# Optimization experiments

Measured on AMD Instinct MI355X. Metric: run time of the kernel, lower is better.

## Reference

```python
import jax, jax.numpy as jnp
import numpy as np

B, S, E = 4, 4096, 128  # batch, seq_len, embedding_dim (quaternion groups)
D = 4 * E               # flattened feature dim fed to the Linear layers


def setup_inputs() -> dict:
    key = jax.random.key(0)
    ks = jax.random.split(key, 9)
    scale_w = 1.0 / np.sqrt(D).astype(np.float32)
    return {
        "query": jax.random.normal(ks[0], (B, S, E, 4), dtype=jnp.float32),
        "key": jax.random.normal(ks[1], (B, S, E, 4), dtype=jnp.float32),
        "value": jax.random.normal(ks[2], (B, S, E, 4), dtype=jnp.float32),
        "Wq": jax.random.normal(ks[3], (D, D), dtype=jnp.float32) * scale_w,
        "bq": jax.random.normal(ks[4], (D,), dtype=jnp.float32) * 0.01,
        "Wk": jax.random.normal(ks[5], (D, D), dtype=jnp.float32) * scale_w,
        "bk": jax.random.normal(ks[6], (D,), dtype=jnp.float32) * 0.01,
        "Wv": jax.random.normal(ks[7], (D, D), dtype=jnp.float32) * scale_w,
        "bv": jax.random.normal(ks[8], (D,), dtype=jnp.float32) * 0.01,
    }


def reference(query, key, value, Wq, bq, Wk, bk, Wv, bv):
    b, s = query.shape[0], query.shape[1]
    e = query.shape[2]  # embedding_dim
    # flatten quaternion dim: [B,S,E,4] -> [B,S,4E]
    q = query.reshape(b, s, -1)
    k = key.reshape(b, key.shape[1], -1)
    v = value.reshape(b, value.shape[1], -1)
    # torch nn.Linear: x @ W^T + bias
    Q = (q @ Wq.T + bq).reshape(b, s, -1, 4)
    K = (k @ Wk.T + bk).reshape(b, key.shape[1], -1, 4)
    V = (v @ Wv.T + bv).reshape(b, value.shape[1], -1, 4)
    # full QK^T over quaternion-grouped dims: [B,S,S]
    scores = jnp.einsum('bseq,bkeq->bsk', Q, K) / jnp.sqrt(jnp.float32(e))
    weights = jax.nn.softmax(scores, axis=-1)
    # faithful to the source: weights are summed over k and scale V at position s
    output = jnp.einsum('bsk,bseq->bseq', weights, V)
    return output, weights
```

## Files before the change

### kernel.cpp

```cpp
#include <hip/hip_runtime.h>
#include <cstdint>

typedef _Float16 h1;
typedef _Float16 h4 __attribute__((ext_vector_type(4)));
typedef _Float16 h8 __attribute__((ext_vector_type(8)));
typedef float    f4 __attribute__((ext_vector_type(4)));
typedef float    f32x4 __attribute__((ext_vector_type(4)));

#define NB 4
#define SL 4096
#define DD 512
#define MM (NB*SL)
#define SHIFT 12.0f

__global__ __launch_bounds__(256) void convert_all(
    const float* __restrict__ Xq, const float* __restrict__ Xk, const float* __restrict__ Xv,
    const float* __restrict__ Wq, const float* __restrict__ Wk, const float* __restrict__ Wv,
    h1* __restrict__ Xh, h1* __restrict__ Wh)
{
    const int xper = MM*DD/4;
    const int wper = DD*DD/4;
    const int xtot = 3*xper;
    int i = blockIdx.x * 256 + threadIdx.x;
    const float* src;
    h1* dst;
    int j;
    if (i < xtot) {
        int mat = i / xper; j = i - mat*xper;
        src = (mat==0) ? Xq : (mat==1 ? Xk : Xv);
        dst = Xh + (size_t)mat*MM*DD;
    } else {
        int t = i - xtot;
        if (t >= 3*wper) return;
        int mat = t / wper; j = t - mat*wper;
        src = (mat==0) ? Wq : (mat==1 ? Wk : Wv);
        dst = Wh + (size_t)mat*DD*DD;
    }
    f4 v = ((const f4*)src)[j];
    h4 hv;
    hv[0]=(h1)v[0]; hv[1]=(h1)v[1]; hv[2]=(h1)v[2]; hv[3]=(h1)v[3];
    ((h4*)dst)[j] = hv;
}

__device__ __forceinline__ void stage_tile(const h1* __restrict__ gbase,
                                           h1* lds, int w, int l)
{
    #pragma unroll
    for (int j = 0; j < 4; j++) {
        const int cc  = w*4 + j;
        const int row = cc*8 + (l >> 3);
        const int sc  = (l & 7) ^ (l >> 3);
        const h1* src = gbase + (size_t)row * DD + sc*8;
        void* dst = (char*)lds + cc*1024;
        __builtin_amdgcn_global_load_lds(
            (const __attribute__((address_space(1))) uint32_t*)src,
            (__attribute__((address_space(3))) uint32_t*)dst, 16, 0, 0);
    }
}

__device__ __forceinline__ h8 lds_frag(const h1* lds, int row, int lc)
{
    const int chunk = lc ^ (row & 7);
    return *(const h8*)(lds + row*64 + chunk*8);
}

__device__ __forceinline__ void stage_slot32(const h1* __restrict__ gbase,
                                             char* ldsbase, int w, int l)
{
    #pragma unroll
    for (int j = 0; j < 2; j++) {
        const int lc  = j*512 + w*64 + l;
        const int row = lc >> 2;
        const int ch  = lc & 3;
        const int sc  = ch ^ ((row >> 1) & 3);
        const h1* src = gbase + (size_t)row * DD + sc*8;
        __builtin_amdgcn_global_load_lds(
            (const __attribute__((address_space(1))) uint32_t*)src,
            (__attribute__((address_space(3))) uint32_t*)(ldsbase + (size_t)(j*512 + w*64)*16),
            16, 0, 0);
    }
}

__device__ __forceinline__ h8 frag32(const h1* lds, int row, int g)
{
    const int ch = g ^ ((row >> 1) & 3);
    return *(const h8*)(lds + row*32 + ch*8);
}

__device__ __forceinline__ void slab_write16(h1* slab, const float (&vals)[4][4], int g, int c)
{
    #pragma unroll
    for (int i = 0; i < 4; i++)
        #pragma unroll
        for (int nf = 0; nf < 4; nf++)
            slab[(g*4+i)*72 + nf*16 + c] = (h1)vals[i][nf];
}

__device__ __forceinline__ void slab_flush(const h1* slab, int lane, h1* gdst0, int grow)
{
    __builtin_amdgcn_wave_barrier();
    asm volatile("s_waitcnt lgkmcnt(0)" ::: "memory");
    const int rl = lane >> 3, ch = lane & 7;
    h8 v0 = *(const h8*)(slab + rl*72 + ch*8);
    h8 v1 = *(const h8*)(slab + (8+rl)*72 + ch*8);
    *(h8*)(gdst0 + (size_t)rl*grow + ch*8)     = v0;
    *(h8*)(gdst0 + (size_t)(8+rl)*grow + ch*8) = v1;
    __builtin_amdgcn_wave_barrier();
}

__global__ __launch_bounds__(256) void proj_gemm(
    const h1* __restrict__ Xh, const h1* __restrict__ Wh,
    const float* __restrict__ bq, const float* __restrict__ bk, const float* __restrict__ bv,
    h1* __restrict__ Qh, h1* __restrict__ Kh, float* __restrict__ Vout)
{
    const int prj = blockIdx.z;
    const h1* __restrict__ X    = Xh + (size_t)prj * MM * DD;
    const h1* __restrict__ W    = Wh + (size_t)prj * DD * DD;
    const float* __restrict__ bias = (prj==0) ? bq : (prj==1 ? bk : bv);

    const int m0 = blockIdx.y * 128;
    const int n0 = blockIdx.x * 128;

    __shared__ h1 As[128*64];
    __shared__ h1 Bs[128*64];

    const int tid  = threadIdx.x;
    const int lane = tid & 63;
    const int wid  = tid >> 6;
    const int wm = wid >> 1, wn = wid & 1;
    const int g  = lane >> 4, c = lane & 15;

    f32x4 acc[4][4];
    #pragma unroll
    for (int i = 0; i < 4; i++)
        #pragma unroll
        for (int j = 0; j < 4; j++) acc[i][j] = (f32x4){0.f, 0.f, 0.f, 0.f};

    for (int k0 = 0; k0 < DD; k0 += 64) {
        __syncthreads();
        stage_tile(X + (size_t)m0 * DD + k0, As, wid, lane);
        stage_tile(W + (size_t)n0 * DD + k0, Bs, wid, lane);
        __syncthreads();
        #pragma unroll
        for (int kk = 0; kk < 2; kk++) {
            h8 af[4], bf[4];
            #pragma unroll
            for (int mf = 0; mf < 4; mf++) af[mf] = lds_frag(As, wm*64 + mf*16 + c, kk*4 + g);
            #pragma unroll
            for (int nf = 0; nf < 4; nf++) bf[nf] = lds_frag(Bs, wn*64 + nf*16 + c, kk*4 + g);
            #pragma unroll
            for (int mf = 0; mf < 4; mf++)
                #pragma unroll
                for (int nf = 0; nf < 4; nf++)
                    acc[mf][nf] = __builtin_amdgcn_mfma_f32_16x16x32_f16(af[mf], bf[nf], acc[mf][nf], 0, 0, 0);
        }
    }

    float bv4[4];
    #pragma unroll
    for (int nf = 0; nf < 4; nf++) bv4[nf] = bias[n0 + wn*64 + nf*16 + c];

    __syncthreads();

    if (prj < 2) {
        h1* dstbase = (prj == 0) ? Qh : Kh;
        h1* slab = As + wid*1152;
        #pragma unroll
        for (int mf = 0; mf < 4; mf++) {
            float vals[4][4];
            #pragma unroll
            for (int i = 0; i < 4; i++)
                #pragma unroll
                for (int nf = 0; nf < 4; nf++)
                    vals[i][nf] = acc[mf][nf][i] + bv4[nf];
            slab_write16(slab, vals, g, c);
            slab_flush(slab, lane,
                       dstbase + (size_t)(m0 + wm*64 + mf*16)*DD + n0 + wn*64, DD);
        }
    } else {
        #pragma unroll
        for (int mf = 0; mf < 4; mf++) {
            #pragma unroll
            for (int i = 0; i < 4; i++) {
                const int row = m0 + wm*64 + mf*16 + g*4 + i;
                #pragma unroll
                for (int nf = 0; nf < 4; nf++) {
                    const int col = n0 + wn*64 + nf*16 + c;
                    Vout[(size_t)row*DD + col] = acc[mf][nf][i] + bv4[nf];
                }
            }
        }
    }
}

__global__ __launch_bounds__(512) void scores_gemm_8ph(
    const h1* __restrict__ Qh, const h1* __restrict__ Kh,
    h1* __restrict__ Eh,
    float* __restrict__ partial)
{
    const int orig = blockIdx.x;
    const int swz  = (orig & 7) * 128 + (orig >> 3);
    const int b  = swz >> 8;
    const int t_ = swz & 255;
    const int ty = t_ >> 4;
    const int tx = t_ & 15;
    const int m0 = ty * 256;
    const int n0 = tx * 256;
    const h1* __restrict__ Qb = Qh + (size_t)b * SL * DD;
    const h1* __restrict__ Kb = Kh + (size_t)b * SL * DD;

    __shared__ h1 Albuf[4*256*32];
    __shared__ h1 Blbuf[4*256*32];
    const int SLOT_H = 256*32;
    const int SLOT_B = SLOT_H*2;

    const int tid  = threadIdx.x;
    const int lane = tid & 63;
    const int wid  = tid >> 6;
    const int wm = wid >> 2;
    const int wn = wid & 3;
    const int g  = lane >> 4, c = lane & 15;

    f32x4 acc[8][4];
    #pragma unroll
    for (int i = 0; i < 8; i++)
        #pragma unroll
        for (int j = 0; j < 4; j++) acc[i][j] = (f32x4){0.f, 0.f, 0.f, 0.f};

    #pragma unroll
    for (int kt = 0; kt < 3; ++kt) {
        stage_slot32(Qb + (size_t)m0*DD + kt*32, (char*)Albuf + kt*SLOT_B, wid, lane);
        stage_slot32(Kb + (size_t)n0*DD + kt*32, (char*)Blbuf + kt*SLOT_B, wid, lane);
    }
    asm volatile("s_waitcnt vmcnt(8)" ::: "memory");
    __builtin_amdgcn_s_barrier();

    for (int kt = 0; kt < 16; ++kt) {
        const int cur = kt & 3;
        const h1* Abase = Albuf + cur*SLOT_H;
        const h1* Bbase = Blbuf + cur*SLOT_H;

        h8 af[4], bf[4];
        #pragma unroll
        for (int fm = 0; fm < 4; fm++) af[fm] = frag32(Abase, wm*128 + fm*16 + c, g);
        #pragma unroll
        for (int fn = 0; fn < 4; fn++) bf[fn] = frag32(Bbase, wn*64 + fn*16 + c, g);

        if (kt <= 12) {
            const int nk = kt + 3, ns = nk & 3;
            stage_slot32(Qb + (size_t)m0*DD + nk*32, (char*)Albuf + ns*SLOT_B, wid, lane);
            stage_slot32(Kb + (size_t)n0*DD + nk*32, (char*)Blbuf + ns*SLOT_B, wid, lane);
        }

        __builtin_amdgcn_s_barrier();
        asm volatile("s_waitcnt lgkmcnt(0)" ::: "memory");
        __builtin_amdgcn_sched_barrier(0);
        __builtin_amdgcn_s_setprio(1);
        #pragma unroll
        for (int fm = 0; fm < 4; fm++)
            #pragma unroll
            for (int fn = 0; fn < 4; fn++)
                acc[fm][fn] = __builtin_amdgcn_mfma_f32_16x16x32_f16(af[fm], bf[fn], acc[fm][fn], 0, 0, 0);
        __builtin_amdgcn_s_setprio(0);
        __builtin_amdgcn_s_barrier();

        #pragma unroll
        for (int fm = 0; fm < 4; fm++) af[fm] = frag32(Abase, wm*128 + 64 + fm*16 + c, g);

        __builtin_amdgcn_s_barrier();
        asm volatile("s_waitcnt lgkmcnt(0)" ::: "memory");
        __builtin_amdgcn_sched_barrier(0);
        __builtin_amdgcn_s_setprio(1);
        #pragma unroll
        for (int fm = 0; fm < 4; fm++)
            #pragma unroll
            for (int fn = 0; fn < 4; fn++)
                acc[4+fm][fn] = __builtin_amdgcn_mfma_f32_16x16x32_f16(af[fm], bf[fn], acc[4+fm][fn], 0, 0, 0);
        __builtin_amdgcn_s_setprio(0);

        if (kt <= 12)      { asm volatile("s_waitcnt vmcnt(8)" ::: "memory"); }
        else if (kt == 13) { asm volatile("s_waitcnt vmcnt(4)" ::: "memory"); }
        else if (kt == 14) { asm volatile("s_waitcnt vmcnt(0)" ::: "memory"); }
        __builtin_amdgcn_s_barrier();
    }

    const float inv_scale = 0.08838834764831845f;
    h1* slab = Albuf + wid*1152;
    #pragma unroll
    for (int mf = 0; mf < 8; mf++) {
        float vals[4][4];
        #pragma unroll
        for (int i = 0; i < 4; i++) {
            const int row = m0 + wm*128 + mf*16 + g*4 + i;
            float rsum = 0.f;
            #pragma unroll
            for (int nf = 0; nf < 4; nf++) {
                float e = __expf(fmaf(acc[mf][nf][i], inv_scale, -SHIFT));
                vals[i][nf] = e;
                rsum += e;
            }
            #pragma unroll
            for (int off = 1; off < 16; off <<= 1) rsum += __shfl_xor(rsum, off);
            if (c == 0)
                partial[((size_t)b * SL + row) * 64 + tx * 4 + wn] = rsum;
        }
        slab_write16(slab, vals, g, c);
        slab_flush(slab, lane,
                   Eh + ((size_t)b * SL + m0 + wm*128 + mf*16) * SL + n0 + wn*64, SL);
    }
}

__global__ __launch_bounds__(256) void rownorm(
    const float* __restrict__ partial, const h1* __restrict__ Eh,
    float* __restrict__ Wout)
{
    const int row = blockIdx.x;
    const int tid = threadIdx.x;
    __shared__ float sinv;
    if (tid < 64) {
        float s = partial[(size_t)row * 64 + tid];
        #pragma unroll
        for (int off = 32; off > 0; off >>= 1) s += __shfl_xor(s, off);
        if (tid == 0) sinv = 1.0f / s;
    }
    __syncthreads();
    const float s = sinv;
    const h8* er = (const h8*)(Eh + (size_t)row * SL);
    f4* wr = (f4*)(Wout + (size_t)row * SL);
    #pragma unroll
    for (int jj = 0; jj < 2; jj++) {
        const int j = tid + jj*256;
        h8 v = er[j];
        f4 o0, o1;
        #pragma unroll
        for (int x = 0; x < 4; x++) { o0[x] = (float)v[x] * s; o1[x] = (float)v[4+x] * s; }
        wr[2*j]   = o0;
        wr[2*j+1] = o1;
    }
}

extern "C" void kernel_launch(void* const* d_in, const int* in_sizes, int n_in,
                              void* d_out, int out_size, void* d_ws, size_t ws_size,
                              hipStream_t stream)
{
    const float* q  = (const float*)d_in[0];
    const float* k  = (const float*)d_in[1];
    const float* v  = (const float*)d_in[2];
    const float* Wq = (const float*)d_in[3];
    const float* bq = (const float*)d_in[4];
    const float* Wk = (const float*)d_in[5];
    const float* bk = (const float*)d_in[6];
    const float* Wv = (const float*)d_in[7];
    const float* bv = (const float*)d_in[8];

    float* out  = (float*)d_out;
    float* Vout = out;
    float* Wout = out + (size_t)MM * DD;

    char* ws = (char*)d_ws;
    h1* Xh = (h1*)ws;
    h1* Wh = (h1*)(ws + (size_t)3*MM*DD*2);
    h1* Qh = (h1*)((char*)Wh + (size_t)3*DD*DD*2);
    h1* Kh = (h1*)((char*)Qh + (size_t)MM*DD*2);
    float* partial = (float*)((char*)Kh + (size_t)MM*DD*2);
    float* invrow  = (float*)((char*)partial + (size_t)MM*64*4);
    h1* Eh = (h1*)((char*)invrow + (size_t)MM*4);

    const int conv_chunks = (3*MM*DD + 3*DD*DD) / 4;
    convert_all<<<(conv_chunks + 255)/256, 256, 0, stream>>>(q, k, v, Wq, Wk, Wv, Xh, Wh);
    proj_gemm<<<dim3(4, 128, 3), 256, 0, stream>>>(Xh, Wh, bq, bk, bv, Qh, Kh, Vout);
    scores_gemm_8ph<<<1024, 512, 0, stream>>>(Qh, Kh, Eh, partial);
    rownorm<<<MM, 256, 0, stream>>>(partial, Eh, Wout);
}
```

Before: 264.9 us.

## Fuse fp32-to-fp16 activation conversion into projection GEMM and merge scores MFMA phases

Drops the separate conversion pass over the three activation tensors. The projection GEMM now loads fp32 inputs directly, converts them in registers and writes them to a padded LDS tile, which avoids writing and re-reading an fp16 copy. Only the weights are still pre-converted. The scores GEMM also loads all eight A fragments at once and runs a single MFMA phase with fewer barriers, at the cost of higher register pressure. The activation loads now go through registers instead of asynchronous global-to-LDS copies, so each projection block re-reads fp32 X four times across the N tiles.

```diff
diff --git a/kernel.cpp b/kernel.cpp
--- a/kernel.cpp
+++ b/kernel.cpp
@@ -13,33 +13,20 @@
 #define MM (NB*SL)
 #define SHIFT 12.0f
 
-__global__ __launch_bounds__(256) void convert_all(
-    const float* __restrict__ Xq, const float* __restrict__ Xk, const float* __restrict__ Xv,
+__global__ __launch_bounds__(256) void convert_w_kernel(
     const float* __restrict__ Wq, const float* __restrict__ Wk, const float* __restrict__ Wv,
-    h1* __restrict__ Xh, h1* __restrict__ Wh)
-{
-    const int xper = MM*DD/4;
-    const int wper = DD*DD/4;
-    const int xtot = 3*xper;
+    h1* __restrict__ Wh)
+{
+    const int per = DD*DD/4;
     int i = blockIdx.x * 256 + threadIdx.x;
-    const float* src;
-    h1* dst;
-    int j;
-    if (i < xtot) {
-        int mat = i / xper; j = i - mat*xper;
-        src = (mat==0) ? Xq : (mat==1 ? Xk : Xv);
-        dst = Xh + (size_t)mat*MM*DD;
-    } else {
-        int t = i - xtot;
-        if (t >= 3*wper) return;
-        int mat = t / wper; j = t - mat*wper;
-        src = (mat==0) ? Wq : (mat==1 ? Wk : Wv);
-        dst = Wh + (size_t)mat*DD*DD;
-    }
+    if (i >= 3*per) return;
+    int mat = i / per;
+    int j = i - mat*per;
+    const float* src = (mat==0) ? Wq : (mat==1 ? Wk : Wv);
     f4 v = ((const f4*)src)[j];
     h4 hv;
     hv[0]=(h1)v[0]; hv[1]=(h1)v[1]; hv[2]=(h1)v[2]; hv[3]=(h1)v[3];
-    ((h4*)dst)[j] = hv;
+    ((h4*)(Wh + (size_t)mat*DD*DD))[j] = hv;
 }
 
 __device__ __forceinline__ void stage_tile(const h1* __restrict__ gbase,
@@ -109,19 +96,20 @@
 }
 
 __global__ __launch_bounds__(256) void proj_gemm(
-    const h1* __restrict__ Xh, const h1* __restrict__ Wh,
+    const float* __restrict__ Xq, const float* __restrict__ Xk, const float* __restrict__ Xv,
+    const h1* __restrict__ Wh,
     const float* __restrict__ bq, const float* __restrict__ bk, const float* __restrict__ bv,
     h1* __restrict__ Qh, h1* __restrict__ Kh, float* __restrict__ Vout)
 {
     const int prj = blockIdx.z;
-    const h1* __restrict__ X    = Xh + (size_t)prj * MM * DD;
-    const h1* __restrict__ W    = Wh + (size_t)prj * DD * DD;
+    const float* __restrict__ X    = (prj==0) ? Xq : (prj==1 ? Xk : Xv);
+    const h1*    __restrict__ W    = Wh + (size_t)prj * DD * DD;
     const float* __restrict__ bias = (prj==0) ? bq : (prj==1 ? bk : bv);
 
     const int m0 = blockIdx.y * 128;
     const int n0 = blockIdx.x * 128;
 
-    __shared__ h1 As[128*64];
+    __shared__ h1 As[128][72];
     __shared__ h1 Bs[128*64];
 
     const int tid  = threadIdx.x;
@@ -129,6 +117,7 @@
     const int wid  = tid >> 6;
     const int wm = wid >> 1, wn = wid & 1;
     const int g  = lane >> 4, c = lane & 15;
+    const int r  = tid >> 1,  h = tid & 1;
 
     f32x4 acc[4][4];
     #pragma unroll
@@ -138,14 +127,31 @@
 
     for (int k0 = 0; k0 < DD; k0 += 64) {
         __syncthreads();
-        stage_tile(X + (size_t)m0 * DD + k0, As, wid, lane);
         stage_tile(W + (size_t)n0 * DD + k0, Bs, wid, lane);
+        {
+            const f4* src = (const f4*)(X + (size_t)(m0 + r) * DD + k0 + h*32);
+            f4 a0=src[0], a1=src[1], a2=src[2], a3=src[3],
+               a4=src[4], a5=src[5], a6=src[6], a7=src[7];
+            h8 p0, p1, p2, p3;
+            #pragma unroll
+            for (int j = 0; j < 4; j++) {
+                p0[j]=(h1)a0[j]; p0[4+j]=(h1)a1[j];
+                p1[j]=(h1)a2[j]; p1[4+j]=(h1)a3[j];
+                p2[j]=(h1)a4[j]; p2[4+j]=(h1)a5[j];
+                p3[j]=(h1)a6[j]; p3[4+j]=(h1)a7[j];
+            }
+            *(h8*)&As[r][h*32]      = p0;
+            *(h8*)&As[r][h*32 + 8]  = p1;
+            *(h8*)&As[r][h*32 + 16] = p2;
+            *(h8*)&As[r][h*32 + 24] = p3;
+        }
         __syncthreads();
+
         #pragma unroll
         for (int kk = 0; kk < 2; kk++) {
             h8 af[4], bf[4];
             #pragma unroll
-            for (int mf = 0; mf < 4; mf++) af[mf] = lds_frag(As, wm*64 + mf*16 + c, kk*4 + g);
+            for (int mf = 0; mf < 4; mf++) af[mf] = *(const h8*)&As[wm*64 + mf*16 + c][kk*32 + g*8];
             #pragma unroll
             for (int nf = 0; nf < 4; nf++) bf[nf] = lds_frag(Bs, wn*64 + nf*16 + c, kk*4 + g);
             #pragma unroll
@@ -164,7 +170,7 @@
 
     if (prj < 2) {
         h1* dstbase = (prj == 0) ? Qh : Kh;
-        h1* slab = As + wid*1152;
+        h1* slab = &As[0][0] + wid*1152;
         #pragma unroll
         for (int mf = 0; mf < 4; mf++) {
             float vals[4][4];
@@ -193,7 +199,7 @@
     }
 }
 
-__global__ __launch_bounds__(512) void scores_gemm_8ph(
+__global__ __launch_bounds__(512) void scores_gemm(
     const h1* __restrict__ Qh, const h1* __restrict__ Kh,
     h1* __restrict__ Eh,
     float* __restrict__ partial)
@@ -240,9 +246,9 @@
         const h1* Abase = Albuf + cur*SLOT_H;
         const h1* Bbase = Blbuf + cur*SLOT_H;
 
-        h8 af[4], bf[4];
-        #pragma unroll
-        for (int fm = 0; fm < 4; fm++) af[fm] = frag32(Abase, wm*128 + fm*16 + c, g);
+        h8 af[8], bf[4];
+        #pragma unroll
+        for (int fm = 0; fm < 8; fm++) af[fm] = frag32(Abase, wm*128 + fm*16 + c, g);
         #pragma unroll
         for (int fn = 0; fn < 4; fn++) bf[fn] = frag32(Bbase, wn*64 + fn*16 + c, g);
 
@@ -252,30 +258,14 @@
             stage_slot32(Kb + (size_t)n0*DD + nk*32, (char*)Blbuf + ns*SLOT_B, wid, lane);
         }
 
-        __builtin_amdgcn_s_barrier();
         asm volatile("s_waitcnt lgkmcnt(0)" ::: "memory");
         __builtin_amdgcn_sched_barrier(0);
         __builtin_amdgcn_s_setprio(1);
         #pragma unroll
-        for (int fm = 0; fm < 4; fm++)
+        for (int fm = 0; fm < 8; fm++)
             #pragma unroll
             for (int fn = 0; fn < 4; fn++)
                 acc[fm][fn] = __builtin_amdgcn_mfma_f32_16x16x32_f16(af[fm], bf[fn], acc[fm][fn], 0, 0, 0);
-        __builtin_amdgcn_s_setprio(0);
-        __builtin_amdgcn_s_barrier();
-
-        #pragma unroll
-        for (int fm = 0; fm < 4; fm++) af[fm] = frag32(Abase, wm*128 + 64 + fm*16 + c, g);
-
-        __builtin_amdgcn_s_barrier();
-        asm volatile("s_waitcnt lgkmcnt(0)" ::: "memory");
-        __builtin_amdgcn_sched_barrier(0);
-        __builtin_amdgcn_s_setprio(1);
-        #pragma unroll
-        for (int fm = 0; fm < 4; fm++)
-            #pragma unroll
-            for (int fn = 0; fn < 4; fn++)
-                acc[4+fm][fn] = __builtin_amdgcn_mfma_f32_16x16x32_f16(af[fm], bf[fn], acc[4+fm][fn], 0, 0, 0);
         __builtin_amdgcn_s_setprio(0);
 
         if (kt <= 12)      { asm volatile("s_waitcnt vmcnt(8)" ::: "memory"); }
@@ -358,17 +348,15 @@
     float* Wout = out + (size_t)MM * DD;
 
     char* ws = (char*)d_ws;
-    h1* Xh = (h1*)ws;
-    h1* Wh = (h1*)(ws + (size_t)3*MM*DD*2);
-    h1* Qh = (h1*)((char*)Wh + (size_t)3*DD*DD*2);
+    h1* Wh = (h1*)ws;
+    h1* Qh = (h1*)(ws + (size_t)3*DD*DD*2);
     h1* Kh = (h1*)((char*)Qh + (size_t)MM*DD*2);
     float* partial = (float*)((char*)Kh + (size_t)MM*DD*2);
     float* invrow  = (float*)((char*)partial + (size_t)MM*64*4);
     h1* Eh = (h1*)((char*)invrow + (size_t)MM*4);
 
-    const int conv_chunks = (3*MM*DD + 3*DD*DD) / 4;
-    convert_all<<<(conv_chunks + 255)/256, 256, 0, stream>>>(q, k, v, Wq, Wk, Wv, Xh, Wh);
-    proj_gemm<<<dim3(4, 128, 3), 256, 0, stream>>>(Xh, Wh, bq, bk, bv, Qh, Kh, Vout);
-    scores_gemm_8ph<<<1024, 512, 0, stream>>>(Qh, Kh, Eh, partial);
+    convert_w_kernel<<<768, 256, 0, stream>>>(Wq, Wk, Wv, Wh);
+    proj_gemm<<<dim3(4, 128, 3), 256, 0, stream>>>(q, k, v, Wh, bq, bk, bv, Qh, Kh, Vout);
+    scores_gemm<<<1024, 512, 0, stream>>>(Qh, Kh, Eh, partial);
     rownorm<<<MM, 256, 0, stream>>>(partial, Eh, Wout);
 }
```

Measured after the change: 276.7 us. 1.04x slower.

## Make scores GEMM persistent over four tiles and stage V output via LDS

Applied to the files above, without the earlier changes.

The scores GEMM now launches 256 blocks, each looping over four consecutive 256x256 tiles, instead of 1024 blocks. The XCD-aware block swizzle is dropped. Separately, the fp32 V projection epilogue is staged through shared memory, so each row is written with coalesced 16-byte stores instead of scattered scalar ones. The persistent loop is meant to cut launch and tail overhead, but it serializes the prologue and epilogue of each tile, and losing the swizzle may reduce L2 reuse.

```diff
diff --git a/kernel.cpp b/kernel.cpp
--- a/kernel.cpp
+++ b/kernel.cpp
@@ -108,6 +108,30 @@
     __builtin_amdgcn_wave_barrier();
 }
 
+__device__ __forceinline__ void slab_write32(float* slab, const float (&vals)[4][4], int g, int c)
+{
+    #pragma unroll
+    for (int i = 0; i < 4; i++)
+        #pragma unroll
+        for (int nf = 0; nf < 4; nf++)
+            slab[(g*4+i)*68 + nf*16 + c] = vals[i][nf];
+}
+
+__device__ __forceinline__ void slab_flush32(const float* slab, int lane, float* gdst0, int grow)
+{
+    __builtin_amdgcn_wave_barrier();
+    asm volatile("s_waitcnt lgkmcnt(0)" ::: "memory");
+    const int rl = lane >> 3, ch = lane & 7;
+    #pragma unroll
+    for (int half = 0; half < 2; half++) {
+        f4 v0 = *(const f4*)(slab + rl*68     + half*32 + ch*4);
+        f4 v1 = *(const f4*)(slab + (8+rl)*68 + half*32 + ch*4);
+        *(f4*)(gdst0 + (size_t)rl*grow     + half*32 + ch*4) = v0;
+        *(f4*)(gdst0 + (size_t)(8+rl)*grow + half*32 + ch*4) = v1;
+    }
+    __builtin_amdgcn_wave_barrier();
+}
+
 __global__ __launch_bounds__(256) void proj_gemm(
     const h1* __restrict__ Xh, const h1* __restrict__ Wh,
     const float* __restrict__ bq, const float* __restrict__ bk, const float* __restrict__ bv,
@@ -178,36 +202,28 @@
                        dstbase + (size_t)(m0 + wm*64 + mf*16)*DD + n0 + wn*64, DD);
         }
     } else {
+        float* slab32 = (float*)((char*)(wid < 2 ? As : Bs) + (wid & 1)*4352);
         #pragma unroll
         for (int mf = 0; mf < 4; mf++) {
-            #pragma unroll
-            for (int i = 0; i < 4; i++) {
-                const int row = m0 + wm*64 + mf*16 + g*4 + i;
-                #pragma unroll
-                for (int nf = 0; nf < 4; nf++) {
-                    const int col = n0 + wn*64 + nf*16 + c;
-                    Vout[(size_t)row*DD + col] = acc[mf][nf][i] + bv4[nf];
-                }
-            }
-        }
-    }
-}
-
-__global__ __launch_bounds__(512) void scores_gemm_8ph(
+            float vals[4][4];
+            #pragma unroll
+            for (int i = 0; i < 4; i++)
+                #pragma unroll
+                for (int nf = 0; nf < 4; nf++)
+                    vals[i][nf] = acc[mf][nf][i] + bv4[nf];
+            slab_write32(slab32, vals, g, c);
+            slab_flush32(slab32, lane,
+                         Vout + (size_t)(m0 + wm*64 + mf*16)*DD + n0 + wn*64, DD);
+        }
+    }
+}
+
+__global__ __launch_bounds__(512) void scores_gemm(
     const h1* __restrict__ Qh, const h1* __restrict__ Kh,
     h1* __restrict__ Eh,
     float* __restrict__ partial)
 {
-    const int orig = blockIdx.x;
-    const int swz  = (orig & 7) * 128 + (orig >> 3);
-    const int b  = swz >> 8;
-    const int t_ = swz & 255;
-    const int ty = t_ >> 4;
-    const int tx = t_ & 15;
-    const int m0 = ty * 256;
-    const int n0 = tx * 256;
-    const h1* __restrict__ Qb = Qh + (size_t)b * SL * DD;
-    const h1* __restrict__ Kb = Kh + (size_t)b * SL * DD;
+    const int bid = blockIdx.x;
 
     __shared__ h1 Albuf[4*256*32];
     __shared__ h1 Blbuf[4*256*32];
@@ -221,92 +237,106 @@
     const int wn = wid & 3;
     const int g  = lane >> 4, c = lane & 15;
 
-    f32x4 acc[8][4];
-    #pragma unroll
-    for (int i = 0; i < 8; i++)
-        #pragma unroll
-        for (int j = 0; j < 4; j++) acc[i][j] = (f32x4){0.f, 0.f, 0.f, 0.f};
-
-    #pragma unroll
-    for (int kt = 0; kt < 3; ++kt) {
-        stage_slot32(Qb + (size_t)m0*DD + kt*32, (char*)Albuf + kt*SLOT_B, wid, lane);
-        stage_slot32(Kb + (size_t)n0*DD + kt*32, (char*)Blbuf + kt*SLOT_B, wid, lane);
-    }
-    asm volatile("s_waitcnt vmcnt(8)" ::: "memory");
-    __builtin_amdgcn_s_barrier();
-
-    for (int kt = 0; kt < 16; ++kt) {
-        const int cur = kt & 3;
-        const h1* Abase = Albuf + cur*SLOT_H;
-        const h1* Bbase = Blbuf + cur*SLOT_H;
-
-        h8 af[4], bf[4];
-        #pragma unroll
-        for (int fm = 0; fm < 4; fm++) af[fm] = frag32(Abase, wm*128 + fm*16 + c, g);
-        #pragma unroll
-        for (int fn = 0; fn < 4; fn++) bf[fn] = frag32(Bbase, wn*64 + fn*16 + c, g);
-
-        if (kt <= 12) {
-            const int nk = kt + 3, ns = nk & 3;
-            stage_slot32(Qb + (size_t)m0*DD + nk*32, (char*)Albuf + ns*SLOT_B, wid, lane);
-            stage_slot32(Kb + (size_t)n0*DD + nk*32, (char*)Blbuf + ns*SLOT_B, wid, lane);
-        }
-
+    #pragma unroll 1
+    for (int tt = 0; tt < 4; tt++) {
+        const int t_ = bid*4 + tt;
+        const int b  = t_ >> 8;
+        const int ty = (t_ >> 4) & 15;
+        const int tx = t_ & 15;
+        const int m0 = ty * 256;
+        const int n0 = tx * 256;
+        const h1* __restrict__ Qb = Qh + (size_t)b * SL * DD;
+        const h1* __restrict__ Kb = Kh + (size_t)b * SL * DD;
+
+        f32x4 acc[8][4];
+        #pragma unroll
+        for (int i = 0; i < 8; i++)
+            #pragma unroll
+            for (int j = 0; j < 4; j++) acc[i][j] = (f32x4){0.f, 0.f, 0.f, 0.f};
+
+        __syncthreads();
+
+        #pragma unroll
+        for (int kt = 0; kt < 3; ++kt) {
+            stage_slot32(Qb + (size_t)m0*DD + kt*32, (char*)Albuf + kt*SLOT_B, wid, lane);
+            stage_slot32(Kb + (size_t)n0*DD + kt*32, (char*)Blbuf + kt*SLOT_B, wid, lane);
+        }
+        asm volatile("s_waitcnt vmcnt(8)" ::: "memory");
         __builtin_amdgcn_s_barrier();
-        asm volatile("s_waitcnt lgkmcnt(0)" ::: "memory");
-        __builtin_amdgcn_sched_barrier(0);
-        __builtin_amdgcn_s_setprio(1);
-        #pragma unroll
-        for (int fm = 0; fm < 4; fm++)
-            #pragma unroll
-            for (int fn = 0; fn < 4; fn++)
-                acc[fm][fn] = __builtin_amdgcn_mfma_f32_16x16x32_f16(af[fm], bf[fn], acc[fm][fn], 0, 0, 0);
-        __builtin_amdgcn_s_setprio(0);
-        __builtin_amdgcn_s_barrier();
-
-        #pragma unroll
-        for (int fm = 0; fm < 4; fm++) af[fm] = frag32(Abase, wm*128 + 64 + fm*16 + c, g);
-
-        __builtin_amdgcn_s_barrier();
-        asm volatile("s_waitcnt lgkmcnt(0)" ::: "memory");
-        __builtin_amdgcn_sched_barrier(0);
-        __builtin_amdgcn_s_setprio(1);
-        #pragma unroll
-        for (int fm = 0; fm < 4; fm++)
-            #pragma unroll
-            for (int fn = 0; fn < 4; fn++)
-                acc[4+fm][fn] = __builtin_amdgcn_mfma_f32_16x16x32_f16(af[fm], bf[fn], acc[4+fm][fn], 0, 0, 0);
-        __builtin_amdgcn_s_setprio(0);
-
-        if (kt <= 12)      { asm volatile("s_waitcnt vmcnt(8)" ::: "memory"); }
-        else if (kt == 13) { asm volatile("s_waitcnt vmcnt(4)" ::: "memory"); }
-        else if (kt == 14) { asm volatile("s_waitcnt vmcnt(0)" ::: "memory"); }
-        __builtin_amdgcn_s_barrier();
-    }
-
-    const float inv_scale = 0.08838834764831845f;
-    h1* slab = Albuf + wid*1152;
-    #pragma unroll
-    for (int mf = 0; mf < 8; mf++) {
-        float vals[4][4];
-        #pragma unroll
-        for (int i = 0; i < 4; i++) {
-            const int row = m0 + wm*128 + mf*16 + g*4 + i;
-            float rsum = 0.f;
-            #pragma unroll
-            for (int nf = 0; nf < 4; nf++) {
-                float e = __expf(fmaf(acc[mf][nf][i], inv_scale, -SHIFT));
-                vals[i][nf] = e;
-                rsum += e;
+
+        for (int kt = 0; kt < 16; ++kt) {
+            const int cur = kt & 3;
+            const h1* Abase = Albuf + cur*SLOT_H;
+            const h1* Bbase = Blbuf + cur*SLOT_H;
+
+            h8 af[4], bf[4];
+            #pragma unroll
+            for (int fm = 0; fm < 4; fm++) af[fm] = frag32(Abase, wm*128 + fm*16 + c, g);
+            #pragma unroll
+            for (int fn = 0; fn < 4; fn++) bf[fn] = frag32(Bbase, wn*64 + fn*16 + c, g);
+
+            if (kt <= 12) {
+                const int nk = kt + 3, ns = nk & 3;
+                stage_slot32(Qb + (size_t)m0*DD + nk*32, (char*)Albuf + ns*SLOT_B, wid, lane);
+                stage_slot32(Kb + (size_t)n0*DD + nk*32, (char*)Blbuf + ns*SLOT_B, wid, lane);
             }
-            #pragma unroll
-            for (int off = 1; off < 16; off <<= 1) rsum += __shfl_xor(rsum, off);
-            if (c == 0)
-                partial[((size_t)b * SL + row) * 64 + tx * 4 + wn] = rsum;
-        }
-        slab_write16(slab, vals, g, c);
-        slab_flush(slab, lane,
-                   Eh + ((size_t)b * SL + m0 + wm*128 + mf*16) * SL + n0 + wn*64, SL);
+
+            __builtin_amdgcn_s_barrier();
+            asm volatile("s_waitcnt lgkmcnt(0)" ::: "memory");
+            __builtin_amdgcn_sched_barrier(0);
+            __builtin_amdgcn_s_setprio(1);
+            #pragma unroll
+            for (int fm = 0; fm < 4; fm++)
+                #pragma unroll
+                for (int fn = 0; fn < 4; fn++)
+                    acc[fm][fn] = __builtin_amdgcn_mfma_f32_16x16x32_f16(af[fm], bf[fn], acc[fm][fn], 0, 0, 0);
+            __builtin_amdgcn_s_setprio(0);
+            __builtin_amdgcn_s_barrier();
+
+            #pragma unroll
+            for (int fm = 0; fm < 4; fm++) af[fm] = frag32(Abase, wm*128 + 64 + fm*16 + c, g);
+
+            __builtin_amdgcn_s_barrier();
+            asm volatile("s_waitcnt lgkmcnt(0)" ::: "memory");
+            __builtin_amdgcn_sched_barrier(0);
+            __builtin_amdgcn_s_setprio(1);
+            #pragma unroll
+            for (int fm = 0; fm < 4; fm++)
+                #pragma unroll
+                for (int fn = 0; fn < 4; fn++)
+                    acc[4+fm][fn] = __builtin_amdgcn_mfma_f32_16x16x32_f16(af[fm], bf[fn], acc[4+fm][fn], 0, 0, 0);
+            __builtin_amdgcn_s_setprio(0);
+
+            if (kt <= 12)      { asm volatile("s_waitcnt vmcnt(8)" ::: "memory"); }
+            else if (kt == 13) { asm volatile("s_waitcnt vmcnt(4)" ::: "memory"); }
+            else if (kt == 14) { asm volatile("s_waitcnt vmcnt(0)" ::: "memory"); }
+            __builtin_amdgcn_s_barrier();
+        }
+
+        const float inv_scale = 0.08838834764831845f;
+        h1* slab = Albuf + wid*1152;
+        #pragma unroll
+        for (int mf = 0; mf < 8; mf++) {
+            float vals[4][4];
+            #pragma unroll
+            for (int i = 0; i < 4; i++) {
+                const int row = m0 + wm*128 + mf*16 + g*4 + i;
+                float rsum = 0.f;
+                #pragma unroll
+                for (int nf = 0; nf < 4; nf++) {
+                    float e = __expf(fmaf(acc[mf][nf][i], inv_scale, -SHIFT));
+                    vals[i][nf] = e;
+                    rsum += e;
+                }
+                #pragma unroll
+                for (int off = 1; off < 16; off <<= 1) rsum += __shfl_xor(rsum, off);
+                if (c == 0)
+                    partial[((size_t)b * SL + row) * 64 + tx * 4 + wn] = rsum;
+            }
+            slab_write16(slab, vals, g, c);
+            slab_flush(slab, lane,
+                       Eh + ((size_t)b * SL + m0 + wm*128 + mf*16) * SL + n0 + wn*64, SL);
+        }
     }
 }
 
@@ -369,6 +399,6 @@
     const int conv_chunks = (3*MM*DD + 3*DD*DD) / 4;
     convert_all<<<(conv_chunks + 255)/256, 256, 0, stream>>>(q, k, v, Wq, Wk, Wv, Xh, Wh);
     proj_gemm<<<dim3(4, 128, 3), 256, 0, stream>>>(Xh, Wh, bq, bk, bv, Qh, Kh, Vout);
-    scores_gemm_8ph<<<1024, 512, 0, stream>>>(Qh, Kh, Eh, partial);
+    scores_gemm<<<256, 512, 0, stream>>>(Qh, Kh, Eh, partial);
     rownorm<<<MM, 256, 0, stream>>>(partial, Eh, Wout);
 }
```

Measured after the change: 282.3 us. 1.07x slower.
